# Performance work log

Measured on AMD Instinct MI355X. Metric: run time of the kernel, lower is better.

## Reference

```python
import jax, jax.numpy as jnp
import numpy as np

EPS = 1e-12  # torch F.normalize eps

def _l2norm(v, axis):
    n = jnp.linalg.norm(v, axis=axis, keepdims=True)
    return v / jnp.maximum(n, EPS)

def setup_inputs() -> dict:
    key = jax.random.key(0)
    k1, k2, k3 = jax.random.split(key, 3)
    N, D, H, W, K = 32, 512, 40, 40, 64
    x = jax.random.normal(k1, (N, D, H, W), dtype=jnp.float32)
    conv_weight = jax.random.normal(k2, (K, D), dtype=jnp.float32) * 0.05
    centroids = jax.random.uniform(k3, (K, D), dtype=jnp.float32)
    return {"x": x, "conv_weight": conv_weight, "centroids": centroids}

def reference(x, conv_weight, centroids):
    N, D, H, W = x.shape
    K = centroids.shape[0]
    # descriptor-wise L2 normalization over channel dim
    x = _l2norm(x, axis=1)
    x_flat = x.reshape(N, D, H * W)                       # [N, D, S]
    # 1x1 conv == per-pixel linear: [K,D] @ [N,D,S] -> [N,K,S]
    logits = jnp.einsum('kd,nds->nks', conv_weight, x_flat)
    soft_assign = jax.nn.softmax(logits, axis=1)          # softmax over clusters
    # vlad[n,k,d] = sum_s a[n,k,s] * (x[n,d,s] - c[k,d])
    #            = (a @ x^T) - (sum_s a) * c   -- two GEMM-like ops, no K-loop
    agg = jnp.einsum('nks,nds->nkd', soft_assign, x_flat)  # [N, K, D]
    a_sum = soft_assign.sum(axis=2)                        # [N, K]
    vlad = agg - a_sum[:, :, None] * centroids[None, :, :]
    # intra-normalization over D, flatten, global L2 normalization
    vlad = _l2norm(vlad, axis=2)
    vlad = vlad.reshape(N, K * D)
    vlad = _l2norm(vlad, axis=1)
    return vlad
```

## Files before the change

kernel.cpp:

```cpp
#include <hip/hip_runtime.h>
#include <math.h>

#define N_ 32
#define D_ 512
#define S_ 1600
#define K_ 64

typedef __attribute__((ext_vector_type(8))) short short8;
typedef __attribute__((ext_vector_type(4))) float f32x4;

static __device__ __forceinline__ short f2bf(float f) {
    unsigned u = __float_as_uint(f);
    u += 0x7fffu + ((u >> 16) & 1u);
    return (short)(u >> 16);
}

__global__ __launch_bounds__(256) void kW(const float* __restrict__ w,
                                          short* __restrict__ w16)
{
    int i4 = (blockIdx.x * 256 + threadIdx.x) * 4;
    float4 v = *(const float4*)&w[i4];
    short4 h = {f2bf(v.x), f2bf(v.y), f2bf(v.z), f2bf(v.w)};
    *(short4*)&w16[i4] = h;
}

__global__ __launch_bounds__(256) void kA(const float* __restrict__ x,
                                          const short* __restrict__ w16,
                                          short* __restrict__ x16,
                                          short* __restrict__ aprime,
                                          float* __restrict__ asum)
{
    __shared__ unsigned Tw[32 * 34];
    __shared__ float pssq[8][32];
    __shared__ float invL[32];
    __shared__ float wred[2][4][32];

    const int tid = threadIdx.x;
    const int n  = blockIdx.x / 50;
    const int s0 = (blockIdx.x % 50) * 32;
    const int wv = tid >> 6;
    const int l  = tid & 63;
    const int lk = l & 15;
    const int q  = l >> 4;
    const int sl = tid & 31;
    const int g0 = tid >> 5;

    const float* xb = x + (size_t)n * D_ * S_ + s0 + sl;
    short* x16b = x16 + (size_t)n * D_ * S_ + s0 + sl;

    f32x4 acc[2];
    acc[0] = (f32x4){0.f, 0.f, 0.f, 0.f};
    acc[1] = (f32x4){0.f, 0.f, 0.f, 0.f};
    float ssl = 0.f;

    for (int dc = 0; dc < D_; dc += 64) {
        __syncthreads();
#pragma unroll
        for (int j = 0; j < 4; ++j) {
            const int r = g0 + 8 * j;
            float v0 = xb[(size_t)(dc + 2 * r) * S_];
            float v1 = xb[(size_t)(dc + 2 * r + 1) * S_];
            ssl += v0 * v0 + v1 * v1;
            unsigned lo = (unsigned short)f2bf(v0);
            unsigned hi = (unsigned short)f2bf(v1);
            Tw[sl * 34 + r] = lo | (hi << 16);
            x16b[(size_t)(dc + 2 * r) * S_]     = (short)lo;
            x16b[(size_t)(dc + 2 * r + 1) * S_] = (short)hi;
        }
        __syncthreads();

        const short* T = (const short*)Tw;
#pragma unroll
        for (int kst = 0; kst < 2; ++kst) {
            short8 af = *(const short8*)&w16[(16 * wv + lk) * D_ + dc + kst * 32 + q * 8];
#pragma unroll
            for (int st = 0; st < 2; ++st) {
                const short* bp = &T[(st * 16 + lk) * 68 + kst * 32 + q * 8];
                short4 b0 = *(const short4*)bp;
                short4 b1 = *(const short4*)(bp + 4);
                short8 bf = {b0.x, b0.y, b0.z, b0.w, b1.x, b1.y, b1.z, b1.w};
                acc[st] = __builtin_amdgcn_mfma_f32_16x16x32_bf16(af, bf, acc[st], 0, 0, 0);
            }
        }
    }

    __syncthreads();
    pssq[g0][sl] = ssl;
    __syncthreads();
    if (tid < 32) {
        float ss = 0.f;
#pragma unroll
        for (int g = 0; g < 8; ++g) ss += pssq[g][tid];
        invL[tid] = 1.0f / fmaxf(sqrtf(ss), 1e-12f);
    }
    __syncthreads();

    float lg[2][4], invv[2];
#pragma unroll
    for (int st = 0; st < 2; ++st) {
        invv[st] = invL[st * 16 + lk];
#pragma unroll
        for (int r = 0; r < 4; ++r) lg[st][r] = acc[st][r] * invv[st];
    }
#pragma unroll
    for (int st = 0; st < 2; ++st) {
        float m = fmaxf(fmaxf(lg[st][0], lg[st][1]), fmaxf(lg[st][2], lg[st][3]));
        m = fmaxf(m, __shfl_xor(m, 16));
        m = fmaxf(m, __shfl_xor(m, 32));
        if (q == 0) wred[0][wv][st * 16 + lk] = m;
    }
    __syncthreads();
    float gm[2];
#pragma unroll
    for (int st = 0; st < 2; ++st) {
        float m = wred[0][0][st * 16 + lk];
        m = fmaxf(m, wred[0][1][st * 16 + lk]);
        m = fmaxf(m, wred[0][2][st * 16 + lk]);
        m = fmaxf(m, wred[0][3][st * 16 + lk]);
        gm[st] = m;
    }
    float e[2][4];
#pragma unroll
    for (int st = 0; st < 2; ++st) {
        float s = 0.f;
#pragma unroll
        for (int r = 0; r < 4; ++r) {
            e[st][r] = __expf(lg[st][r] - gm[st]);
            s += e[st][r];
        }
        s += __shfl_xor(s, 16);
        s += __shfl_xor(s, 32);
        if (q == 0) wred[1][wv][st * 16 + lk] = s;
    }
    __syncthreads();
    float rs[2];
#pragma unroll
    for (int st = 0; st < 2; ++st) {
        float s = wred[1][0][st * 16 + lk] + wred[1][1][st * 16 + lk]
                + wred[1][2][st * 16 + lk] + wred[1][3][st * 16 + lk];
        rs[st] = 1.0f / s;
    }

    short* apb = aprime + (size_t)n * K_ * S_ + s0;
#pragma unroll
    for (int r = 0; r < 4; ++r) {
        const int k = 16 * wv + 4 * q + r;
        float accp = 0.f;
#pragma unroll
        for (int st = 0; st < 2; ++st) {
            float p = e[st][r] * rs[st];
            apb[(size_t)k * S_ + st * 16 + lk] = f2bf(p * invv[st]);
            accp += p;
        }
        accp += __shfl_xor(accp, 1);
        accp += __shfl_xor(accp, 2);
        accp += __shfl_xor(accp, 4);
        accp += __shfl_xor(accp, 8);
        if (lk == 0) atomicAdd(&asum[n * K_ + k], accp);
    }
}

__global__ __launch_bounds__(256) void kB(const short* __restrict__ x16,
                                          const short* __restrict__ aprime,
                                          float* __restrict__ aggp)
{
    const int bid = blockIdx.x;
    const int n  = bid / 40;
    const int dt = (bid % 40) / 10;
    const int sp = bid % 10;
    const int wv = threadIdx.x >> 6;
    const int l  = threadIdx.x & 63;
    const int lk = l & 15;
    const int q  = l >> 4;
    const int dbase = dt * 128 + wv * 32;

    const short* ap = aprime + (size_t)n * K_ * S_;
    const short* xb = x16 + (size_t)n * D_ * S_;

    f32x4 acc[4][2];
#pragma unroll
    for (int kt = 0; kt < 4; ++kt)
#pragma unroll
        for (int ds = 0; ds < 2; ++ds) acc[kt][ds] = (f32x4){0.f, 0.f, 0.f, 0.f};

#pragma unroll
    for (int kst = 0; kst < 5; ++kst) {
        const int s = sp * 160 + kst * 32 + q * 8;
        short8 af[4];
#pragma unroll
        for (int kt = 0; kt < 4; ++kt)
            af[kt] = *(const short8*)&ap[(size_t)(kt * 16 + lk) * S_ + s];
        short8 bf[2];
#pragma unroll
        for (int ds = 0; ds < 2; ++ds)
            bf[ds] = *(const short8*)&xb[(size_t)(dbase + ds * 16 + lk) * S_ + s];
#pragma unroll
        for (int kt = 0; kt < 4; ++kt)
#pragma unroll
            for (int ds = 0; ds < 2; ++ds)
                acc[kt][ds] = __builtin_amdgcn_mfma_f32_16x16x32_bf16(af[kt], bf[ds], acc[kt][ds], 0, 0, 0);
    }

    float* ab = aggp + ((size_t)sp * N_ + n) * K_ * D_;
#pragma unroll
    for (int kt = 0; kt < 4; ++kt)
#pragma unroll
        for (int ds = 0; ds < 2; ++ds)
#pragma unroll
            for (int r = 0; r < 4; ++r)
                ab[(size_t)(kt * 16 + 4 * q + r) * D_ + dbase + ds * 16 + lk] = acc[kt][ds][r];
}

__global__ __launch_bounds__(256) void kC(const float* __restrict__ aggp,
                                          const float* __restrict__ asum,
                                          const float* __restrict__ cent,
                                          float* __restrict__ out)
{
    __shared__ float red[4];
    const int tid = threadIdx.x;
    const int nk = blockIdx.x;
    const int k = nk & 63;
    const float as = asum[nk];
    const float* cb = cent + (size_t)k * D_;

    float v0 = 0.f, v1 = 0.f;
#pragma unroll
    for (int p = 0; p < 10; ++p) {
        const float* ag = aggp + (size_t)p * N_ * K_ * D_ + (size_t)nk * D_;
        v0 += ag[tid];
        v1 += ag[tid + 256];
    }
    v0 -= as * cb[tid];
    v1 -= as * cb[tid + 256];
    float ssq = v0 * v0 + v1 * v1;

    ssq += __shfl_xor(ssq, 32);
    ssq += __shfl_xor(ssq, 16);
    ssq += __shfl_xor(ssq, 8);
    ssq += __shfl_xor(ssq, 4);
    ssq += __shfl_xor(ssq, 2);
    ssq += __shfl_xor(ssq, 1);
    if ((tid & 63) == 0) red[tid >> 6] = ssq;
    __syncthreads();
    const float total = red[0] + red[1] + red[2] + red[3];
    const float scale = 1.0f / (fmaxf(sqrtf(total), 1e-12f) * 8.0f);

    out[(size_t)nk * D_ + tid]       = v0 * scale;
    out[(size_t)nk * D_ + tid + 256] = v1 * scale;
}

extern "C" void kernel_launch(void* const* d_in, const int* in_sizes, int n_in,
                              void* d_out, int out_size, void* d_ws, size_t ws_size,
                              hipStream_t stream)
{
    const float* x    = (const float*)d_in[0];
    const float* w    = (const float*)d_in[1];
    const float* cent = (const float*)d_in[2];
    float* out = (float*)d_out;

    float* aggp   = (float*)d_ws;
    float* asum   = aggp + (size_t)10 * N_ * K_ * D_;
    short* aprime = (short*)(asum + N_ * K_);
    short* w16    = aprime + (size_t)N_ * K_ * S_;
    short* x16    = w16 + (size_t)K_ * D_;

    hipMemsetAsync(asum, 0, (size_t)N_ * K_ * sizeof(float), stream);

    kW<<<32, 256, 0, stream>>>(w, w16);
    kA<<<N_ * (S_ / 32), 256, 0, stream>>>(x, w16, x16, aprime, asum);
    kB<<<N_ * 4 * 10, 256, 0, stream>>>(x16, aprime, aggp);
    kC<<<N_ * K_, 256, 0, stream>>>(aggp, asum, cent, out);
}
```

Before: 211.5 us.

## Split fp32-to-bf16 conversion and norm computation into separate kernel before logits

Moves the conversion of x to bf16 and the per-pixel inverse L2 norm into a new kernel kX that streams x with coalesced 64-wide rows. kA then reads the bf16 copy and the precomputed inverse norms instead of reading fp32 x and reducing sums of squares itself. This is meant to relieve kA of heavy fp32 loads and the extra synchronisation for the norm reduction. In exchange it adds a kernel launch and an extra read of x16 (half the size of x), which raises total memory traffic.

```diff
diff --git a/kernel.cpp b/kernel.cpp
--- a/kernel.cpp
+++ b/kernel.cpp
@@ -24,15 +24,42 @@
     *(short4*)&w16[i4] = h;
 }
 
-__global__ __launch_bounds__(256) void kA(const float* __restrict__ x,
+__global__ __launch_bounds__(256) void kX(const float* __restrict__ x,
+                                          short* __restrict__ x16,
+                                          float* __restrict__ inv)
+{
+    __shared__ float pssq[4][64];
+    const int tid = threadIdx.x;
+    const int n  = blockIdx.x / 25;
+    const int s0 = (blockIdx.x % 25) * 64;
+    const int sx = tid & 63;
+    const int dg = tid >> 6;
+
+    const float* xb = x + (size_t)n * D_ * S_ + s0 + sx;
+    short* ob = x16 + (size_t)n * D_ * S_ + s0 + sx;
+
+    float ss = 0.f;
+#pragma unroll 8
+    for (int r = dg; r < D_; r += 4) {
+        float v = xb[(size_t)r * S_];
+        ss += v * v;
+        ob[(size_t)r * S_] = f2bf(v);
+    }
+    pssq[dg][sx] = ss;
+    __syncthreads();
+    if (tid < 64) {
+        float t = pssq[0][tid] + pssq[1][tid] + pssq[2][tid] + pssq[3][tid];
+        inv[(size_t)n * S_ + s0 + tid] = 1.0f / fmaxf(sqrtf(t), 1e-12f);
+    }
+}
+
+__global__ __launch_bounds__(256) void kA(const short* __restrict__ x16,
                                           const short* __restrict__ w16,
-                                          short* __restrict__ x16,
+                                          const float* __restrict__ inv,
                                           short* __restrict__ aprime,
                                           float* __restrict__ asum)
 {
-    __shared__ unsigned Tw[32 * 34];
-    __shared__ float pssq[8][32];
-    __shared__ float invL[32];
+    __shared__ short T[32 * 68];
     __shared__ float wred[2][4][32];
 
     const int tid = threadIdx.x;
@@ -42,34 +69,26 @@
     const int l  = tid & 63;
     const int lk = l & 15;
     const int q  = l >> 4;
-    const int sl = tid & 31;
-    const int g0 = tid >> 5;
-
-    const float* xb = x + (size_t)n * D_ * S_ + s0 + sl;
-    short* x16b = x16 + (size_t)n * D_ * S_ + s0 + sl;
+    const int s2 = (tid & 15) * 2;
+    const int rr = tid >> 4;
+
+    const short* xb = x16 + (size_t)n * D_ * S_ + s0;
 
     f32x4 acc[2];
     acc[0] = (f32x4){0.f, 0.f, 0.f, 0.f};
     acc[1] = (f32x4){0.f, 0.f, 0.f, 0.f};
-    float ssl = 0.f;
 
     for (int dc = 0; dc < D_; dc += 64) {
         __syncthreads();
 #pragma unroll
         for (int j = 0; j < 4; ++j) {
-            const int r = g0 + 8 * j;
-            float v0 = xb[(size_t)(dc + 2 * r) * S_];
-            float v1 = xb[(size_t)(dc + 2 * r + 1) * S_];
-            ssl += v0 * v0 + v1 * v1;
-            unsigned lo = (unsigned short)f2bf(v0);
-            unsigned hi = (unsigned short)f2bf(v1);
-            Tw[sl * 34 + r] = lo | (hi << 16);
-            x16b[(size_t)(dc + 2 * r) * S_]     = (short)lo;
-            x16b[(size_t)(dc + 2 * r + 1) * S_] = (short)hi;
+            const int row = rr + 16 * j;
+            unsigned pv = *(const unsigned*)&xb[(size_t)(dc + row) * S_ + s2];
+            T[s2 * 68 + row]       = (short)(pv & 0xffffu);
+            T[(s2 + 1) * 68 + row] = (short)(pv >> 16);
         }
         __syncthreads();
 
-        const short* T = (const short*)Tw;
 #pragma unroll
         for (int kst = 0; kst < 2; ++kst) {
             short8 af = *(const short8*)&w16[(16 * wv + lk) * D_ + dc + kst * 32 + q * 8];
@@ -84,21 +103,10 @@
         }
     }
 
-    __syncthreads();
-    pssq[g0][sl] = ssl;
-    __syncthreads();
-    if (tid < 32) {
-        float ss = 0.f;
-#pragma unroll
-        for (int g = 0; g < 8; ++g) ss += pssq[g][tid];
-        invL[tid] = 1.0f / fmaxf(sqrtf(ss), 1e-12f);
-    }
-    __syncthreads();
-
     float lg[2][4], invv[2];
 #pragma unroll
     for (int st = 0; st < 2; ++st) {
-        invv[st] = invL[st * 16 + lk];
+        invv[st] = inv[(size_t)n * S_ + s0 + st * 16 + lk];
 #pragma unroll
         for (int r = 0; r < 4; ++r) lg[st][r] = acc[st][r] * invv[st];
     }
@@ -260,14 +268,16 @@
 
     float* aggp   = (float*)d_ws;
     float* asum   = aggp + (size_t)10 * N_ * K_ * D_;
-    short* aprime = (short*)(asum + N_ * K_);
+    float* invb   = asum + (size_t)N_ * K_;
+    short* aprime = (short*)(invb + (size_t)N_ * S_);
     short* w16    = aprime + (size_t)N_ * K_ * S_;
     short* x16    = w16 + (size_t)K_ * D_;
 
     hipMemsetAsync(asum, 0, (size_t)N_ * K_ * sizeof(float), stream);
 
     kW<<<32, 256, 0, stream>>>(w, w16);
-    kA<<<N_ * (S_ / 32), 256, 0, stream>>>(x, w16, x16, aprime, asum);
+    kX<<<N_ * (S_ / 64), 256, 0, stream>>>(x, x16, invb);
+    kA<<<N_ * (S_ / 32), 256, 0, stream>>>(x16, w16, invb, aprime, asum);
     kB<<<N_ * 4 * 10, 256, 0, stream>>>(x16, aprime, aggp);
     kC<<<N_ * K_, 256, 0, stream>>>(aggp, asum, cent, out);
 }
```

After: 227.4 us. 7.5% more time.
